# Kernel tuning notes

Measured on AMD Instinct MI355X. Metric: run time of the kernel, lower is better.

Reference implementation:

```python
import jax, jax.numpy as jnp
import numpy as np

N_NODES = 100000
N_EDGES = 3200000
D_IN = 128
D_OUT = 128


def setup_inputs() -> dict:
    key = jax.random.key(0)
    k1, k2, k3, k4, k5, k6 = jax.random.split(key, 6)
    x = jax.random.normal(k1, (N_NODES, D_IN), dtype=jnp.float32)
    edge_row = jax.random.randint(k2, (N_EDGES,), 0, N_NODES)  # destination (adj row)
    edge_col = jax.random.randint(k3, (N_EDGES,), 0, N_NODES)  # source (adj col)
    edge_vals = jax.random.uniform(k4, (N_EDGES,), dtype=jnp.float32)
    stdv = 1.0 / np.sqrt(D_OUT)
    weight = jax.random.uniform(k5, (D_IN, D_OUT), dtype=jnp.float32, minval=-stdv, maxval=stdv)
    bias_param = jax.random.uniform(k6, (D_OUT,), dtype=jnp.float32, minval=-stdv, maxval=stdv)
    return {"x": x, "edge_row": edge_row, "edge_col": edge_col,
            "edge_vals": edge_vals, "weight": weight, "bias_param": bias_param}


def reference(x, edge_row, edge_col, edge_vals, weight, bias_param):
    # support = X @ W  : [N, D_OUT]
    support = x @ weight
    # output = spmm(adj, support): out[r] += v * support[c] for each edge (r, c, v)
    messages = edge_vals[:, None] * support[edge_col]  # [E, D_OUT]
    output = jax.ops.segment_sum(messages, edge_row, num_segments=N_NODES)
    return output + bias_param
```

## Files before the change

kernel.cpp:

```cpp
#include <hip/hip_runtime.h>

typedef unsigned int u32;
typedef unsigned long long u64;
typedef unsigned short u16;
typedef unsigned char u8;

#define NN 100000
#define NE 3200000
#define DIM 128
#define RB 256
#define NBK 391
#define BCAP 9216
#define EB 4096

#define OFF_OFFS 0
#define OFF_WB 400064
#define OFF_BCUR 432832
#define OFF_CVP 434432
#define OFF_SH 13234432
#define SCV_BYTES 14417664

typedef __attribute__((ext_vector_type(8))) short bf16x8;
typedef __attribute__((ext_vector_type(4))) float f32x4;

__device__ __forceinline__ float bflo(u32 b) { return __uint_as_float(b << 16); }
__device__ __forceinline__ float bfhi(u32 b) { return __uint_as_float(b & 0xffff0000u); }
__device__ __forceinline__ u16 f2bf(float f) {
    u32 u = __float_as_uint(f);
    return (u16)((u + 0x7fffu + ((u >> 16) & 1u)) >> 16);
}

__global__ __launch_bounds__(256) void bin_kernel(const int4* __restrict__ erow4,
                                                  const int4* __restrict__ ecol4,
                                                  const float4* __restrict__ ev4,
                                                  int* __restrict__ bcur,
                                                  u32* __restrict__ scv,
                                                  u8* __restrict__ slr,
                                                  const float* __restrict__ wf,
                                                  uint4* __restrict__ wB4) {
    __shared__ u32 sscv[EB];
    __shared__ u32 skey[EB];
    __shared__ int sa[512], sb[512], rs[512];
    __shared__ int base[NBK], lcur[NBK];
    int t = threadIdx.x;
    int gid = blockIdx.x * 256 + t;
    if (gid < 2048) {
        int tile = gid >> 6, l = gid & 63;
        int kt = tile >> 3, n = tile & 7;
        int col = n * 16 + (l & 15);
        int kb = kt * 32 + (l >> 4) * 8;
        u32 wp[4];
#pragma unroll
        for (int jj = 0; jj < 4; ++jj) {
            float w0 = wf[(kb + 2 * jj) * DIM + col];
            float w1 = wf[(kb + 2 * jj + 1) * DIM + col];
            wp[jj] = (u32)f2bf(w0) | ((u32)f2bf(w1) << 16);
        }
        wB4[tile * 64 + l] = make_uint4(wp[0], wp[1], wp[2], wp[3]);
    }
    int e0 = blockIdx.x * EB;
    int nval = min(EB, NE - e0);
    int4 er[4];
    bool val[4];
#pragma unroll
    for (int k = 0; k < 4; ++k) {
        int idx4 = (e0 >> 2) + k * 256 + t;
        val[k] = idx4 < NE / 4;
        er[k] = val[k] ? erow4[idx4] : make_int4(0, 0, 0, 0);
    }
    for (int i = t; i < 512; i += 256) sa[i] = 0;
    __syncthreads();
#pragma unroll
    for (int k = 0; k < 4; ++k) {
        if (val[k]) {
            atomicAdd(&sa[er[k].x >> 8], 1);
            atomicAdd(&sa[er[k].y >> 8], 1);
            atomicAdd(&sa[er[k].z >> 8], 1);
            atomicAdd(&sa[er[k].w >> 8], 1);
        }
    }
    __syncthreads();
    for (int i = t; i < NBK; i += 256) base[i] = atomicAdd(&bcur[i], sa[i]);
    int* pa = sa; int* pb = sb;
    for (int d = 1; d < 512; d <<= 1) {
        for (int i = t; i < 512; i += 256)
            pb[i] = (i >= d) ? (pa[i] + pa[i - d]) : pa[i];
        __syncthreads();
        int* tmp = pa; pa = pb; pb = tmp;
    }
    for (int i = t; i < 512; i += 256) {
        int ex = i ? pa[i - 1] : 0;
        rs[i] = ex;
        if (i < NBK) lcur[i] = ex;
    }
    __syncthreads();
#pragma unroll
    for (int k = 0; k < 4; ++k) {
        if (val[k]) {
            int idx4 = (e0 >> 2) + k * 256 + t;
            int4 c = ecol4[idx4];
            float4 v = ev4[idx4];
            int r, b, pos;
            r = er[k].x; b = r >> 8; pos = atomicAdd(&lcur[b], 1);
            sscv[pos] = ((u32)f2bf(v.x) << 17) | (u32)c.x; skey[pos] = ((u32)b << 8) | (u32)(r & 255);
            r = er[k].y; b = r >> 8; pos = atomicAdd(&lcur[b], 1);
            sscv[pos] = ((u32)f2bf(v.y) << 17) | (u32)c.y; skey[pos] = ((u32)b << 8) | (u32)(r & 255);
            r = er[k].z; b = r >> 8; pos = atomicAdd(&lcur[b], 1);
            sscv[pos] = ((u32)f2bf(v.z) << 17) | (u32)c.z; skey[pos] = ((u32)b << 8) | (u32)(r & 255);
            r = er[k].w; b = r >> 8; pos = atomicAdd(&lcur[b], 1);
            sscv[pos] = ((u32)f2bf(v.w) << 17) | (u32)c.w; skey[pos] = ((u32)b << 8) | (u32)(r & 255);
        }
    }
    __syncthreads();
    for (int i = t; i < nval; i += 256) {
        u32 key = skey[i];
        int bk = key >> 8;
        int gl = base[bk] + (i - rs[bk]);
        if (gl < BCAP) {
            scv[bk * BCAP + gl] = sscv[i];
            slr[bk * BCAP + gl] = (u8)(key & 255);
        }
    }
}

__global__ __launch_bounds__(256) void csr_kernel(const u32* __restrict__ scv,
                                                  const u8* __restrict__ slr,
                                                  const int* __restrict__ bcur,
                                                  int* __restrict__ offs,
                                                  u32* __restrict__ cvp) {
    __shared__ u32 lcv[BCAP];
    __shared__ int sa[RB], sb[RB], lcur[RB], red[256];
    int b = blockIdx.x, t = threadIdx.x;
    int r0 = b * RB;
    int rows = min(RB, NN - r0);
    int n = min(bcur[b], BCAP);
    int p = 0;
    for (int i = t; i < b; i += 256) p += min(bcur[i], BCAP);
    red[t] = p;
    sa[t] = 0;
    __syncthreads();
    for (int d = 128; d; d >>= 1) {
        if (t < d) red[t] += red[t + d];
        __syncthreads();
    }
    int gbase = red[0];
    if (b == NBK - 1 && t == 0) offs[NN] = gbase + n;
    const u32* scvB = scv + (size_t)b * BCAP;
    const u8* slrB = slr + (size_t)b * BCAP;
    for (int i = t; i < n; i += 256) atomicAdd(&sa[slrB[i]], 1);
    __syncthreads();
    int* pa = sa; int* pb = sb;
    for (int d = 1; d < 256; d <<= 1) {
        pb[t] = (t >= d) ? (pa[t] + pa[t - d]) : pa[t];
        __syncthreads();
        int* tmp = pa; pa = pb; pb = tmp;
    }
    int excl = t ? pa[t - 1] : 0;
    if (t < rows) offs[r0 + t] = gbase + excl;
    lcur[t] = excl;
    __syncthreads();
    for (int i = t; i < n; i += 256) {
        u32 cv = scvB[i];
        int lr = slrB[i];
        int pos = atomicAdd(&lcur[lr], 1);
        lcv[pos] = cv;
    }
    __syncthreads();
    for (int i = t; i < n; i += 256) cvp[gbase + i] = lcv[i];
}

__global__ __launch_bounds__(256) void gemm_kernel(const float4* __restrict__ xf4,
                                                   const uint4* __restrict__ wB4,
                                                   u32* __restrict__ sup) {
    __shared__ u32 st[64][68];
    int t = threadIdx.x, wave = t >> 6, lane = t & 63;
    int l15 = lane & 15, kg = lane >> 4;
    int row = blockIdx.x * 64 + wave * 16 + l15;
    int rc = min(row, NN - 1);
    f32x4 acc[8];
#pragma unroll
    for (int n = 0; n < 8; ++n) acc[n] = (f32x4){0.f, 0.f, 0.f, 0.f};
#pragma unroll
    for (int kt = 0; kt < 4; ++kt) {
        int k0 = kt * 32 + kg * 8;
        int bidx = (rc * DIM + k0) >> 2;
        float4 xa = xf4[bidx];
        float4 xc = xf4[bidx + 1];
        union { u32 u[4]; bf16x8 v; } A;
        A.u[0] = (u32)f2bf(xa.x) | ((u32)f2bf(xa.y) << 16);
        A.u[1] = (u32)f2bf(xa.z) | ((u32)f2bf(xa.w) << 16);
        A.u[2] = (u32)f2bf(xc.x) | ((u32)f2bf(xc.y) << 16);
        A.u[3] = (u32)f2bf(xc.z) | ((u32)f2bf(xc.w) << 16);
#pragma unroll
        for (int n = 0; n < 8; ++n) {
            union { uint4 u; bf16x8 v; } B;
            B.u = wB4[(kt * 8 + n) * 64 + lane];
            acc[n] = __builtin_amdgcn_mfma_f32_16x16x32_bf16(A.v, B.v, acc[n], 0, 0, 0);
        }
    }
    u16* stp = (u16*)st;
    int rbase = wave * 16 + kg * 4;
#pragma unroll
    for (int n = 0; n < 8; ++n)
#pragma unroll
        for (int i = 0; i < 4; ++i)
            stp[(rbase + i) * 136 + n * 16 + l15] = f2bf(acc[n][i]);
    __syncthreads();
    int r0 = blockIdx.x * 64;
    int rmax = min(64, NN - r0);
    for (int idx = t; idx < 4096; idx += 256) {
        int r = idx >> 6, c = idx & 63;
        if (r < rmax) sup[(r0 + r) * 64 + c] = st[r][c];
    }
}

template <int Q>
__device__ __forceinline__ void gstep(u32 pv, int kk, const u32* __restrict__ sup,
                                      int lane, float& a0, float& a1) {
    u32 ps[Q], xr[Q];
#pragma unroll
    for (int q = 0; q < Q; ++q)
        ps[q] = (u32)__builtin_amdgcn_readlane((int)pv, kk + q);
#pragma unroll
    for (int q = 0; q < Q; ++q)
        xr[q] = __hip_atomic_load(sup + ((ps[q] & 0x1ffffu) << 6) + lane,
                                  __ATOMIC_RELAXED, __HIP_MEMORY_SCOPE_AGENT);
#pragma unroll
    for (int q = 0; q < Q; ++q) {
        float v = bflo(ps[q] >> 17);
        a0 = fmaf(v, bflo(xr[q]), a0);
        a1 = fmaf(v, bfhi(xr[q]), a1);
    }
}

__global__ __launch_bounds__(64) void fused_kernel(const int* __restrict__ offs,
                                                   const u32* __restrict__ cvp,
                                                   const u32* __restrict__ sup,
                                                   const float2* __restrict__ bf2v,
                                                   u64* __restrict__ out) {
    int lane = threadIdx.x;
    int gw = blockIdx.x;
    int start = offs[gw];
    int end = offs[gw + 1];
    int cnt = end - start;
    float2 bp = bf2v[lane];
    float a0 = bp.x, a1 = bp.y;
    for (int j = 0; j < cnt; j += 64) {
        u32 pv = (j + lane < cnt) ? __builtin_nontemporal_load(&cvp[start + j + lane]) : 0u;
        int rem = min(64, cnt - j);
        int kk = 0;
        for (; kk + 32 <= rem; kk += 32) gstep<32>(pv, kk, sup, lane, a0, a1);
        for (; kk < rem; kk += 8) gstep<8>(pv, kk, sup, lane, a0, a1);
    }
    u64 bits = (u64)__float_as_uint(a0) | ((u64)__float_as_uint(a1) << 32);
    __builtin_nontemporal_store(bits, &out[gw * 64 + lane]);
}

extern "C" void kernel_launch(void* const* d_in, const int* in_sizes, int n_in,
                              void* d_out, int out_size, void* d_ws, size_t ws_size,
                              hipStream_t stream) {
    const float* x = (const float*)d_in[0];
    const int* erow = (const int*)d_in[1];
    const int* ecol = (const int*)d_in[2];
    const float* ev = (const float*)d_in[3];
    const float* wf = (const float*)d_in[4];
    const float2* bf2v = (const float2*)d_in[5];

    char* ws = (char*)d_ws;
    int* offs = (int*)(ws + OFF_OFFS);
    uint4* wB4 = (uint4*)(ws + OFF_WB);
    int* bcur = (int*)(ws + OFF_BCUR);
    u32* cvp = (u32*)(ws + OFF_CVP);
    u32* scv = (u32*)(ws + OFF_SH);
    u8* slr = (u8*)(ws + OFF_SH + SCV_BYTES);
    u32* sup = (u32*)(ws + OFF_SH);

    hipMemsetAsync(bcur, 0, NBK * sizeof(int), stream);

    bin_kernel<<<(NE + EB - 1) / EB, 256, 0, stream>>>((const int4*)erow, (const int4*)ecol,
                                                       (const float4*)ev, bcur,
                                                       scv, slr, wf, wB4);
    csr_kernel<<<NBK, 256, 0, stream>>>(scv, slr, bcur, offs, cvp);
    gemm_kernel<<<(NN + 63) / 64, 256, 0, stream>>>((const float4*)x, wB4, sup);
    fused_kernel<<<NN, 64, 0, stream>>>(offs, cvp, sup, bf2v, (u64*)d_out);
}
```

Measured before the change: 309.1 us.

## Slice support matrix by feature chunks and split SpMM across slices

```diff
diff --git a/kernel.cpp b/kernel.cpp
--- a/kernel.cpp
+++ b/kernel.cpp
@@ -12,6 +12,7 @@
 #define NBK 391
 #define BCAP 9216
 #define EB 4096
+#define SLN (NN * 8)
 
 #define OFF_OFFS 0
 #define OFF_WB 400064
@@ -210,50 +211,50 @@
     int rmax = min(64, NN - r0);
     for (int idx = t; idx < 4096; idx += 256) {
         int r = idx >> 6, c = idx & 63;
-        if (r < rmax) sup[(r0 + r) * 64 + c] = st[r][c];
-    }
-}
-
-template <int Q>
-__device__ __forceinline__ void gstep(u32 pv, int kk, const u32* __restrict__ sup,
-                                      int lane, float& a0, float& a1) {
-    u32 ps[Q], xr[Q];
-#pragma unroll
-    for (int q = 0; q < Q; ++q)
-        ps[q] = (u32)__builtin_amdgcn_readlane((int)pv, kk + q);
-#pragma unroll
-    for (int q = 0; q < Q; ++q)
-        xr[q] = __hip_atomic_load(sup + ((ps[q] & 0x1ffffu) << 6) + lane,
-                                  __ATOMIC_RELAXED, __HIP_MEMORY_SCOPE_AGENT);
-#pragma unroll
-    for (int q = 0; q < Q; ++q) {
-        float v = bflo(ps[q] >> 17);
-        a0 = fmaf(v, bflo(xr[q]), a0);
-        a1 = fmaf(v, bfhi(xr[q]), a1);
-    }
-}
-
-__global__ __launch_bounds__(64) void fused_kernel(const int* __restrict__ offs,
-                                                   const u32* __restrict__ cvp,
-                                                   const u32* __restrict__ sup,
-                                                   const float2* __restrict__ bf2v,
-                                                   u64* __restrict__ out) {
-    int lane = threadIdx.x;
-    int gw = blockIdx.x;
-    int start = offs[gw];
-    int end = offs[gw + 1];
-    int cnt = end - start;
-    float2 bp = bf2v[lane];
-    float a0 = bp.x, a1 = bp.y;
-    for (int j = 0; j < cnt; j += 64) {
-        u32 pv = (j + lane < cnt) ? __builtin_nontemporal_load(&cvp[start + j + lane]) : 0u;
-        int rem = min(64, cnt - j);
-        int kk = 0;
-        for (; kk + 32 <= rem; kk += 32) gstep<32>(pv, kk, sup, lane, a0, a1);
-        for (; kk < rem; kk += 8) gstep<8>(pv, kk, sup, lane, a0, a1);
-    }
-    u64 bits = (u64)__float_as_uint(a0) | ((u64)__float_as_uint(a1) << 32);
-    __builtin_nontemporal_store(bits, &out[gw * 64 + lane]);
+        if (r < rmax) sup[(c >> 3) * SLN + (r0 + r) * 8 + (c & 7)] = st[r][c];
+    }
+}
+
+__global__ __launch_bounds__(256) void fused_kernel(const int* __restrict__ offs,
+                                                    const u32* __restrict__ cvp,
+                                                    const u32* __restrict__ sup,
+                                                    const float2* __restrict__ bf2v,
+                                                    u64* __restrict__ out) {
+    int t = threadIdx.x;
+    int wave = t >> 6, lane = t & 63;
+    int bid = blockIdx.x;
+    int s = bid & 7;
+    int node = (bid >> 3) * 4 + wave;
+    int e8 = lane >> 3, j = lane & 7;
+    const u32* sups = sup + s * SLN;
+    int start = offs[node];
+    int cnt = offs[node + 1] - start;
+    float a0 = 0.f, a1 = 0.f;
+    for (int base = 0; base < cnt; base += 64) {
+        u32 pv = (base + lane < cnt) ? __builtin_nontemporal_load(&cvp[start + base + lane]) : 0u;
+        int rem = min(64, cnt - base);
+#pragma unroll 2
+        for (int k = 0; k < rem; k += 8) {
+            int src = k + e8;
+            u32 p = (u32)__shfl((int)pv, src & 63);
+            if (src >= rem) p = 0;
+            u32 xr = __hip_atomic_load(sups + (p & 0x1ffffu) * 8 + j,
+                                       __ATOMIC_RELAXED, __HIP_MEMORY_SCOPE_AGENT);
+            float v = bflo(p >> 17);
+            a0 = fmaf(v, bflo(xr), a0);
+            a1 = fmaf(v, bfhi(xr), a1);
+        }
+    }
+#pragma unroll
+    for (int m = 8; m < 64; m <<= 1) {
+        a0 += __shfl_xor(a0, m);
+        a1 += __shfl_xor(a1, m);
+    }
+    if (lane < 8) {
+        float2 bp = bf2v[s * 8 + j];
+        u64 bits = (u64)__float_as_uint(a0 + bp.x) | ((u64)__float_as_uint(a1 + bp.y) << 32);
+        __builtin_nontemporal_store(bits, &out[(size_t)node * 64 + s * 8 + j]);
+    }
 }
 
 extern "C" void kernel_launch(void* const* d_in, const int* in_sizes, int n_in,
@@ -282,5 +283,5 @@
                                                        scv, slr, wf, wB4);
     csr_kernel<<<NBK, 256, 0, stream>>>(scv, slr, bcur, offs, cvp);
     gemm_kernel<<<(NN + 63) / 64, 256, 0, stream>>>((const float4*)x, wB4, sup);
-    fused_kernel<<<NN, 64, 0, stream>>>(offs, cvp, sup, bf2v, (u64*)d_out);
-}
+    fused_kernel<<<(NN / 4) * 8, 256, 0, stream>>>(offs, cvp, sup, bf2v, (u64*)d_out);
+}
```

New measurement: 515.2 us. 1.67x slower.
